# Performance work log

Measured on AMD Instinct MI355X. Metric: run time of the kernel, lower is better.

## Reference

```python
import jax, jax.numpy as jnp
import numpy as np

N_NODES = 100000
N_EDGES = 1600000
IN_DIM = 128
HEADS = 8
NEG_SLOPE = 0.2  # PyG GATConv default


def _glorot(key, shape):
    fan_in, fan_out = shape[0], shape[-1]
    lim = jnp.sqrt(6.0 / (fan_in + fan_out))
    return jax.random.uniform(key, shape, jnp.float32, -lim, lim)


def setup_inputs() -> dict:
    key = jax.random.key(0)
    ks = jax.random.split(key, 20)
    x = jax.random.normal(ks[0], (N_NODES, IN_DIM), jnp.float32)
    edge_index = jax.random.randint(ks[1], (2, N_EDGES), 0, N_NODES, jnp.int32)
    # layer 1: 128 -> 8 heads x 16
    W1 = _glorot(ks[2], (128, 128)); a_src1 = _glorot(ks[3], (8, 16)); a_dst1 = _glorot(ks[4], (8, 16)); b1 = jnp.zeros((128,), jnp.float32)
    # layer 2: 128 -> 8 heads x 16
    W2 = _glorot(ks[5], (128, 128)); a_src2 = _glorot(ks[6], (8, 16)); a_dst2 = _glorot(ks[7], (8, 16)); b2 = jnp.zeros((128,), jnp.float32)
    # layer 3: 128 -> 1 head x 64, concat=False (mean)
    W3 = _glorot(ks[8], (128, 64)); a_src3 = _glorot(ks[9], (1, 64)); a_dst3 = _glorot(ks[10], (1, 64)); b3 = jnp.zeros((64,), jnp.float32)
    Wout = _glorot(ks[11], (64, 2)); bout = jnp.zeros((2,), jnp.float32)
    return {"x": x, "edge_index": edge_index,
            "W1": W1, "a_src1": a_src1, "a_dst1": a_dst1, "b1": b1,
            "W2": W2, "a_src2": a_src2, "a_dst2": a_dst2, "b2": b2,
            "W3": W3, "a_src3": a_src3, "a_dst3": a_dst3, "b3": b3,
            "Wout": Wout, "bout": bout}


def gat_conv(x, src, dst, W, a_src, a_dst, bias, concat):
    """PyG-style GATConv (eval mode, self-loops already appended to src/dst)."""
    n = x.shape[0]
    H, C = a_src.shape
    h = (x @ W).reshape(n, H, C)                        # [N,H,C]
    alpha_src = jnp.einsum('nhc,hc->nh', h, a_src)       # [N,H]
    alpha_dst = jnp.einsum('nhc,hc->nh', h, a_dst)       # [N,H]
    e = jax.nn.leaky_relu(alpha_src[src] + alpha_dst[dst], NEG_SLOPE)  # [E,H]
    # segment softmax over incoming edges of each destination node
    m = jax.ops.segment_max(e, dst, num_segments=n)      # [N,H]
    ex = jnp.exp(e - m[dst])
    denom = jax.ops.segment_sum(ex, dst, num_segments=n)  # [N,H]
    alpha = ex / (denom[dst] + 1e-16)                    # [E,H]
    # weighted gather-scatter aggregation
    msg = alpha[:, :, None] * h[src]                     # [E,H,C]
    out = jax.ops.segment_sum(msg, dst, num_segments=n)  # [N,H,C]
    out = out.reshape(n, H * C) if concat else out.mean(axis=1)
    return out + bias


def reference(x, edge_index, W1, a_src1, a_dst1, b1, W2, a_src2, a_dst2, b2,
              W3, a_src3, a_dst3, b3, Wout, bout):
    n = x.shape[0]
    loops = jnp.arange(n, dtype=edge_index.dtype)
    src = jnp.concatenate([edge_index[0], loops])
    dst = jnp.concatenate([edge_index[1], loops])
    h = jax.nn.elu(gat_conv(x, src, dst, W1, a_src1, a_dst1, b1, concat=True))
    h = jax.nn.elu(gat_conv(h, src, dst, W2, a_src2, a_dst2, b2, concat=True))
    h = jax.nn.elu(gat_conv(h, src, dst, W3, a_src3, a_dst3, b3, concat=False))
    return h @ Wout + bout
```

## Files before the change

kernel.cpp:

```cpp
#include <hip/hip_runtime.h>
#include <math.h>

#define NN 100000
#define NE 1600000
#define ET (NE + NN)
#define SCAN_BLK 4096

__device__ inline unsigned short f2bf(float f) {
  union { float f; unsigned u; } v; v.f = f;
  unsigned r = v.u + 0x7fffu + ((v.u >> 16) & 1u);
  return (unsigned short)(r >> 16);
}
__device__ inline float bflo(unsigned u) { union { unsigned u; float f; } v; v.u = u << 16; return v.f; }
__device__ inline float bfhi(unsigned u) { union { unsigned u; float f; } v; v.u = u & 0xffff0000u; return v.f; }

__global__ __launch_bounds__(256) void k_hist(const int* __restrict__ dst, int* __restrict__ counts,
                                              int* __restrict__ slots) {
  int i = blockIdx.x * 256 + threadIdx.x;
  if (i >= ET) return;
  int d = (i < NE) ? dst[i] : (i - NE);
  slots[i] = atomicAdd(&counts[d], 1);
}

__global__ __launch_bounds__(256) void k_scan1(const int* __restrict__ counts, int* __restrict__ partial,
                                               int* __restrict__ blksum) {
  __shared__ int lds[256];
  int b = blockIdx.x, t = threadIdx.x;
  int base = b * SCAN_BLK + t * 16;
  int v[16];
  int s = 0;
#pragma unroll
  for (int j = 0; j < 16; j++) {
    int x = (base + j < NN) ? counts[base + j] : 0;
    s += x; v[j] = s;
  }
  lds[t] = s; __syncthreads();
  int tot = s;
  for (int off = 1; off < 256; off <<= 1) {
    int u = 0; if (t >= off) u = lds[t - off];
    __syncthreads(); lds[t] += u; __syncthreads();
  }
  int pre = lds[t] - tot;
#pragma unroll
  for (int j = 0; j < 16; j++) if (base + j < NN) partial[base + j] = pre + v[j];
  if (t == 255) blksum[b] = lds[255];
}

__global__ __launch_bounds__(256) void k_scan2(int* __restrict__ blksum, int nb) {
  __shared__ int lds[256];
  int t = threadIdx.x;
  int v = (t < nb) ? blksum[t] : 0;
  lds[t] = v; __syncthreads();
  for (int off = 1; off < 256; off <<= 1) {
    int u = 0; if (t >= off) u = lds[t - off];
    __syncthreads(); lds[t] += u; __syncthreads();
  }
  if (t < nb) blksum[t] = lds[t] - v;
}

__global__ __launch_bounds__(256) void k_scan3(const int* __restrict__ partial, const int* __restrict__ blksum,
                                               int* __restrict__ rowptr) {
  int i = blockIdx.x * 256 + threadIdx.x;
  if (i >= NN) return;
  rowptr[i + 1] = partial[i] + blksum[i / SCAN_BLK];
  if (i == 0) rowptr[0] = 0;
}

__global__ __launch_bounds__(256) void k_scatter(const int* __restrict__ src, const int* __restrict__ dst,
                                                 const int* __restrict__ rowptr, const int* __restrict__ slots,
                                                 int* __restrict__ esrc) {
  int i = blockIdx.x * 256 + threadIdx.x;
  if (i >= ET) return;
  int d, s;
  if (i < NE) { d = dst[i]; s = src[i]; } else { d = i - NE; s = d; }
  esrc[rowptr[d] + slots[i]] = s;
}

template<int M, bool XBF>
__global__ __launch_bounds__(256) void k_gemm(const float* __restrict__ Xf, const unsigned short* __restrict__ Xb,
                                              const float* __restrict__ W,
                                              const float* __restrict__ a_src, const float* __restrict__ a_dst,
                                              unsigned short* __restrict__ Hf, float* __restrict__ as_, float* __restrict__ ad_) {
  constexpr int CPT = M / 16;
  __shared__ float xs[64 * 36];
  __shared__ float ws[32 * M];
  const int t = threadIdx.x;
  const int tx = t & 15, ty = t >> 4;
  const int row0 = blockIdx.x * 64;
  const int c0 = tx * CPT;
  float acc[4][CPT];
#pragma unroll
  for (int i = 0; i < 4; i++)
#pragma unroll
    for (int j = 0; j < CPT; j++) acc[i][j] = 0.f;

  for (int st = 0; st < 4; ++st) {
    const int k0 = st * 32;
    __syncthreads();
    if constexpr (!XBF) {
#pragma unroll
      for (int j = 0; j < 2; ++j) {
        int flat = t + j * 256;
        int r = flat >> 3, c4 = (flat & 7) * 4;
        float4 v = make_float4(0.f, 0.f, 0.f, 0.f);
        if (row0 + r < NN) v = *(const float4*)(Xf + (size_t)(row0 + r) * 128 + k0 + c4);
        *(float4*)(xs + r * 36 + c4) = v;
      }
    } else {
      int r = t >> 2, c8 = (t & 3) * 8;
      uint4 v = make_uint4(0, 0, 0, 0);
      if (row0 + r < NN) v = *(const uint4*)(Xb + (size_t)(row0 + r) * 128 + k0 + c8);
      float* d = xs + r * 36 + c8;
      d[0] = bflo(v.x); d[1] = bfhi(v.x); d[2] = bflo(v.y); d[3] = bfhi(v.y);
      d[4] = bflo(v.z); d[5] = bfhi(v.z); d[6] = bflo(v.w); d[7] = bfhi(v.w);
    }
#pragma unroll
    for (int j = 0; j < M / 32; ++j) {
      int flat = t + j * 256;
      int r = flat / (M / 4), c4 = (flat % (M / 4)) * 4;
      *(float4*)(ws + r * M + c4) = *(const float4*)(W + (size_t)(k0 + r) * M + c4);
    }
    __syncthreads();
#pragma unroll
    for (int kk = 0; kk < 32; kk += 4) {
      float4 xv[4];
#pragma unroll
      for (int i = 0; i < 4; ++i) xv[i] = *(const float4*)(xs + (ty * 4 + i) * 36 + kk);
#pragma unroll
      for (int j = 0; j < 4; ++j) {
#pragma unroll
        for (int cc = 0; cc < CPT; cc += 4) {
          float4 wv = *(const float4*)(ws + (kk + j) * M + c0 + cc);
#pragma unroll
          for (int i = 0; i < 4; ++i) {
            float xx = ((const float*)&xv[i])[j];
            acc[i][cc + 0] += xx * wv.x;
            acc[i][cc + 1] += xx * wv.y;
            acc[i][cc + 2] += xx * wv.z;
            acc[i][cc + 3] += xx * wv.w;
          }
        }
      }
    }
  }

  float s1[4], s2[4];
#pragma unroll
  for (int i = 0; i < 4; ++i) {
    float a = 0.f, b = 0.f;
#pragma unroll
    for (int j = 0; j < CPT; ++j) { a += acc[i][j] * a_src[c0 + j]; b += acc[i][j] * a_dst[c0 + j]; }
    s1[i] = a; s2[i] = b;
  }
  if constexpr (M == 128) {
#pragma unroll
    for (int i = 0; i < 4; ++i) { s1[i] += __shfl_xor(s1[i], 1); s2[i] += __shfl_xor(s2[i], 1); }
  } else {
#pragma unroll
    for (int off = 1; off < 16; off <<= 1)
#pragma unroll
      for (int i = 0; i < 4; ++i) { s1[i] += __shfl_xor(s1[i], off); s2[i] += __shfl_xor(s2[i], off); }
  }
#pragma unroll
  for (int i = 0; i < 4; ++i) {
    int r = row0 + ty * 4 + i;
    if (r < NN) {
      if constexpr (M == 128) {
        uint4 pk;
        pk.x = (unsigned)f2bf(acc[i][0]) | ((unsigned)f2bf(acc[i][1]) << 16);
        pk.y = (unsigned)f2bf(acc[i][2]) | ((unsigned)f2bf(acc[i][3]) << 16);
        pk.z = (unsigned)f2bf(acc[i][4]) | ((unsigned)f2bf(acc[i][5]) << 16);
        pk.w = (unsigned)f2bf(acc[i][6]) | ((unsigned)f2bf(acc[i][7]) << 16);
        *(uint4*)(Hf + (size_t)r * M + c0) = pk;
        if ((tx & 1) == 0) { as_[r * 8 + (tx >> 1)] = s1[i]; ad_[r * 8 + (tx >> 1)] = s2[i]; }
      } else {
        uint2 pk;
        pk.x = (unsigned)f2bf(acc[i][0]) | ((unsigned)f2bf(acc[i][1]) << 16);
        pk.y = (unsigned)f2bf(acc[i][2]) | ((unsigned)f2bf(acc[i][3]) << 16);
        *(uint2*)(Hf + (size_t)r * M + c0) = pk;
        if (tx == 0) { as_[r] = s1[i]; ad_[r] = s2[i]; }
      }
    }
  }
}

template<int HH, int C, bool FINAL>
__global__ __launch_bounds__(256) void k_aggregate(const unsigned short* __restrict__ Hf, const float* __restrict__ as_,
                                                   const float* __restrict__ ad_, const int* __restrict__ rowptr,
                                                   const int* __restrict__ esrc, const float* __restrict__ bias,
                                                   const float* __restrict__ Wout, const float* __restrict__ bout,
                                                   unsigned short* __restrict__ outb, float* __restrict__ outf) {
  constexpr int CT = HH * C;
  constexpr int Q = CT / 4;
  int g = blockIdx.x * 256 + threadIdx.x;
  if (g >= NN * Q) return;
  int node = g / Q;
  int q = g - node * Q;
  int c = q * 4;
  int hh = c / C;
  int i0 = rowptr[node], i1 = rowptr[node + 1];
  float ad = ad_[node * HH + hh];
  float m0 = -INFINITY, d0 = 0.f;
  float m1 = -INFINITY, d1 = 0.f;
  float4 a0 = make_float4(0.f, 0.f, 0.f, 0.f);
  float4 a1 = make_float4(0.f, 0.f, 0.f, 0.f);
  int i = i0;
  for (; i + 1 < i1; i += 2) {
    int sA = esrc[i], sB = esrc[i + 1];
    float eA = as_[sA * HH + hh] + ad;
    float eB = as_[sB * HH + hh] + ad;
    uint2 hA = *(const uint2*)(Hf + (size_t)sA * CT + c);
    uint2 hB = *(const uint2*)(Hf + (size_t)sB * CT + c);
    eA = fmaxf(eA, 0.2f * eA);
    eB = fmaxf(eB, 0.2f * eB);
    float nmA = fmaxf(m0, eA), nmB = fmaxf(m1, eB);
    float scA = __expf(m0 - nmA), scB = __expf(m1 - nmB);
    float pA = __expf(eA - nmA), pB = __expf(eB - nmB);
    d0 = d0 * scA + pA;                 d1 = d1 * scB + pB;
    a0.x = a0.x * scA + pA * bflo(hA.x); a1.x = a1.x * scB + pB * bflo(hB.x);
    a0.y = a0.y * scA + pA * bfhi(hA.x); a1.y = a1.y * scB + pB * bfhi(hB.x);
    a0.z = a0.z * scA + pA * bflo(hA.y); a1.z = a1.z * scB + pB * bflo(hB.y);
    a0.w = a0.w * scA + pA * bfhi(hA.y); a1.w = a1.w * scB + pB * bfhi(hB.y);
    m0 = nmA; m1 = nmB;
  }
  if (i < i1) {
    int sA = esrc[i];
    float eA = as_[sA * HH + hh] + ad;
    uint2 hA = *(const uint2*)(Hf + (size_t)sA * CT + c);
    eA = fmaxf(eA, 0.2f * eA);
    float nmA = fmaxf(m0, eA);
    float scA = __expf(m0 - nmA);
    float pA = __expf(eA - nmA);
    d0 = d0 * scA + pA;
    a0.x = a0.x * scA + pA * bflo(hA.x);
    a0.y = a0.y * scA + pA * bfhi(hA.x);
    a0.z = a0.z * scA + pA * bflo(hA.y);
    a0.w = a0.w * scA + pA * bfhi(hA.y);
    m0 = nmA;
  }
  float mm = fmaxf(m0, m1);
  float s0 = __expf(m0 - mm), s1v = __expf(m1 - mm);
  float den = d0 * s0 + d1 * s1v;
  float4 acc;
  acc.x = a0.x * s0 + a1.x * s1v;
  acc.y = a0.y * s0 + a1.y * s1v;
  acc.z = a0.z * s0 + a1.z * s1v;
  acc.w = a0.w * s0 + a1.w * s1v;

  float inv = 1.f / den;
  float4 o;
  o.x = acc.x * inv + bias[c + 0];
  o.y = acc.y * inv + bias[c + 1];
  o.z = acc.z * inv + bias[c + 2];
  o.w = acc.w * inv + bias[c + 3];
  o.x = o.x > 0.f ? o.x : __expf(o.x) - 1.f;
  o.y = o.y > 0.f ? o.y : __expf(o.y) - 1.f;
  o.z = o.z > 0.f ? o.z : __expf(o.z) - 1.f;
  o.w = o.w > 0.f ? o.w : __expf(o.w) - 1.f;
  if constexpr (!FINAL) {
    uint2 pk;
    pk.x = (unsigned)f2bf(o.x) | ((unsigned)f2bf(o.y) << 16);
    pk.y = (unsigned)f2bf(o.z) | ((unsigned)f2bf(o.w) << 16);
    *(uint2*)(outb + (size_t)node * CT + c) = pk;
  } else {
    float p0 = o.x * Wout[(c + 0) * 2 + 0] + o.y * Wout[(c + 1) * 2 + 0]
             + o.z * Wout[(c + 2) * 2 + 0] + o.w * Wout[(c + 3) * 2 + 0];
    float p1 = o.x * Wout[(c + 0) * 2 + 1] + o.y * Wout[(c + 1) * 2 + 1]
             + o.z * Wout[(c + 2) * 2 + 1] + o.w * Wout[(c + 3) * 2 + 1];
#pragma unroll
    for (int off = 1; off < 16; off <<= 1) { p0 += __shfl_xor(p0, off); p1 += __shfl_xor(p1, off); }
    if (q == 0) { outf[node * 2 + 0] = p0 + bout[0]; outf[node * 2 + 1] = p1 + bout[1]; }
  }
}

extern "C" void kernel_launch(void* const* d_in, const int* in_sizes, int n_in,
                              void* d_out, int out_size, void* d_ws, size_t ws_size,
                              hipStream_t stream) {
  const float* x    = (const float*)d_in[0];
  const int*   ei   = (const int*)d_in[1];
  const float* W1   = (const float*)d_in[2];
  const float* as1  = (const float*)d_in[3];
  const float* ad1  = (const float*)d_in[4];
  const float* b1   = (const float*)d_in[5];
  const float* W2   = (const float*)d_in[6];
  const float* as2  = (const float*)d_in[7];
  const float* ad2  = (const float*)d_in[8];
  const float* b2   = (const float*)d_in[9];
  const float* W3   = (const float*)d_in[10];
  const float* as3  = (const float*)d_in[11];
  const float* ad3  = (const float*)d_in[12];
  const float* b3   = (const float*)d_in[13];
  const float* Wout = (const float*)d_in[14];
  const float* bout = (const float*)d_in[15];
  const int* srcp = ei;
  const int* dstp = ei + NE;

  char* p = (char*)d_ws;
  auto alloc = [&](size_t bytes) { char* r = p; p += (bytes + 255) & ~size_t(255); return r; };
  int*            rowptr  = (int*)alloc((size_t)(NN + 1) * 4);
  int*            counts  = (int*)alloc((size_t)NN * 4);
  int*            partial = (int*)alloc((size_t)NN * 4);
  int*            blksum  = (int*)alloc(256 * 4);
  int*            esrc    = (int*)alloc((size_t)ET * 4);
  int*            slots   = (int*)alloc((size_t)ET * 4);
  float*          asb     = (float*)alloc((size_t)NN * 8 * 4);
  float*          adb     = (float*)alloc((size_t)NN * 8 * 4);
  unsigned short* hfb     = (unsigned short*)alloc((size_t)NN * 128 * 2);
  unsigned short* actb    = (unsigned short*)alloc((size_t)NN * 128 * 2);

  hipMemsetAsync(counts, 0, (size_t)NN * 4, stream);
  int gE = (ET + 255) / 256;
  int nb = (NN + SCAN_BLK - 1) / SCAN_BLK;
  k_hist<<<gE, 256, 0, stream>>>(dstp, counts, slots);
  k_scan1<<<nb, 256, 0, stream>>>(counts, partial, blksum);
  k_scan2<<<1, 256, 0, stream>>>(blksum, nb);
  k_scan3<<<(NN + 255) / 256, 256, 0, stream>>>(partial, blksum, rowptr);
  k_scatter<<<gE, 256, 0, stream>>>(srcp, dstp, rowptr, slots, esrc);

  int gGemm = (NN + 63) / 64;
  k_gemm<128, false><<<gGemm, 256, 0, stream>>>(x, nullptr, W1, as1, ad1, hfb, asb, adb);
  k_aggregate<8, 16, false><<<(NN * 32 + 255) / 256, 256, 0, stream>>>(hfb, asb, adb, rowptr, esrc, b1, nullptr, nullptr, actb, nullptr);
  k_gemm<128, true><<<gGemm, 256, 0, stream>>>(nullptr, actb, W2, as2, ad2, hfb, asb, adb);
  k_aggregate<8, 16, false><<<(NN * 32 + 255) / 256, 256, 0, stream>>>(hfb, asb, adb, rowptr, esrc, b2, nullptr, nullptr, actb, nullptr);
  k_gemm<64, true><<<gGemm, 256, 0, stream>>>(nullptr, actb, W3, as3, ad3, hfb, asb, adb);
  k_aggregate<1, 64, true><<<(NN * 16 + 255) / 256, 256, 0, stream>>>(hfb, asb, adb, rowptr, esrc, b3, Wout, bout, nullptr, (float*)d_out);
}
```

Before: 466.0 us.

## Precompute softmax numerators and inverse denominators in separate per-head kernel

Adds a k_mden kernel that computes, per destination node and head, the segment max and the denominator, and stores the unnormalized exp weights per edge in bf16 along with the inverse denominator. The aggregation kernel then only gathers features and does plain FMAs, with no online-softmax rescaling or redundant exp work across the lanes of a head. In exchange it adds an extra launch per layer, a two-pass edge traversal, and a per-edge alpha buffer write and read. Storing alpha in bf16 also lowers precision.

```diff
diff --git a/kernel.cpp b/kernel.cpp
--- a/kernel.cpp
+++ b/kernel.cpp
@@ -13,6 +13,7 @@
 }
 __device__ inline float bflo(unsigned u) { union { unsigned u; float f; } v; v.u = u << 16; return v.f; }
 __device__ inline float bfhi(unsigned u) { union { unsigned u; float f; } v; v.u = u & 0xffff0000u; return v.f; }
+__device__ inline float bfs(unsigned short u) { union { unsigned u; float f; } v; v.u = ((unsigned)u) << 16; return v.f; }
 
 __global__ __launch_bounds__(256) void k_hist(const int* __restrict__ dst, int* __restrict__ counts,
                                               int* __restrict__ slots) {
@@ -184,10 +185,41 @@
   }
 }
 
+template<int HH>
+__global__ __launch_bounds__(256) void k_mden(const float* __restrict__ as_, const float* __restrict__ ad_,
+                                              const int* __restrict__ rowptr, const int* __restrict__ esrc,
+                                              unsigned short* __restrict__ alpha, float* __restrict__ invd) {
+  int g = blockIdx.x * 256 + threadIdx.x;
+  if (g >= NN * HH) return;
+  int node = g / HH;
+  int h = g - node * HH;
+  int i0 = rowptr[node], i1 = rowptr[node + 1];
+  float ad = ad_[g];
+  float m = -INFINITY;
+  for (int i = i0; i < i1; ++i) {
+    int s = esrc[i];
+    float e = as_[s * HH + h] + ad;
+    e = fmaxf(e, 0.2f * e);
+    m = fmaxf(m, e);
+  }
+  float den = 0.f;
+  for (int i = i0; i < i1; ++i) {
+    int s = esrc[i];
+    float e = as_[s * HH + h] + ad;
+    e = fmaxf(e, 0.2f * e);
+    float p = __expf(e - m);
+    den += p;
+    alpha[(size_t)i * HH + h] = f2bf(p);
+  }
+  invd[g] = 1.f / den;
+}
+
 template<int HH, int C, bool FINAL>
-__global__ __launch_bounds__(256) void k_aggregate(const unsigned short* __restrict__ Hf, const float* __restrict__ as_,
-                                                   const float* __restrict__ ad_, const int* __restrict__ rowptr,
-                                                   const int* __restrict__ esrc, const float* __restrict__ bias,
+__global__ __launch_bounds__(256) void k_aggregate(const unsigned short* __restrict__ Hf,
+                                                   const unsigned short* __restrict__ alpha,
+                                                   const float* __restrict__ invd,
+                                                   const int* __restrict__ rowptr, const int* __restrict__ esrc,
+                                                   const float* __restrict__ bias,
                                                    const float* __restrict__ Wout, const float* __restrict__ bout,
                                                    unsigned short* __restrict__ outb, float* __restrict__ outf) {
   constexpr int CT = HH * C;
@@ -199,60 +231,35 @@
   int c = q * 4;
   int hh = c / C;
   int i0 = rowptr[node], i1 = rowptr[node + 1];
-  float ad = ad_[node * HH + hh];
-  float m0 = -INFINITY, d0 = 0.f;
-  float m1 = -INFINITY, d1 = 0.f;
   float4 a0 = make_float4(0.f, 0.f, 0.f, 0.f);
   float4 a1 = make_float4(0.f, 0.f, 0.f, 0.f);
   int i = i0;
   for (; i + 1 < i1; i += 2) {
     int sA = esrc[i], sB = esrc[i + 1];
-    float eA = as_[sA * HH + hh] + ad;
-    float eB = as_[sB * HH + hh] + ad;
+    float pA = bfs(alpha[(size_t)i * HH + hh]);
+    float pB = bfs(alpha[(size_t)(i + 1) * HH + hh]);
     uint2 hA = *(const uint2*)(Hf + (size_t)sA * CT + c);
     uint2 hB = *(const uint2*)(Hf + (size_t)sB * CT + c);
-    eA = fmaxf(eA, 0.2f * eA);
-    eB = fmaxf(eB, 0.2f * eB);
-    float nmA = fmaxf(m0, eA), nmB = fmaxf(m1, eB);
-    float scA = __expf(m0 - nmA), scB = __expf(m1 - nmB);
-    float pA = __expf(eA - nmA), pB = __expf(eB - nmB);
-    d0 = d0 * scA + pA;                 d1 = d1 * scB + pB;
-    a0.x = a0.x * scA + pA * bflo(hA.x); a1.x = a1.x * scB + pB * bflo(hB.x);
-    a0.y = a0.y * scA + pA * bfhi(hA.x); a1.y = a1.y * scB + pB * bfhi(hB.x);
-    a0.z = a0.z * scA + pA * bflo(hA.y); a1.z = a1.z * scB + pB * bflo(hB.y);
-    a0.w = a0.w * scA + pA * bfhi(hA.y); a1.w = a1.w * scB + pB * bfhi(hB.y);
-    m0 = nmA; m1 = nmB;
+    a0.x = fmaf(pA, bflo(hA.x), a0.x);  a1.x = fmaf(pB, bflo(hB.x), a1.x);
+    a0.y = fmaf(pA, bfhi(hA.x), a0.y);  a1.y = fmaf(pB, bfhi(hB.x), a1.y);
+    a0.z = fmaf(pA, bflo(hA.y), a0.z);  a1.z = fmaf(pB, bflo(hB.y), a1.z);
+    a0.w = fmaf(pA, bfhi(hA.y), a0.w);  a1.w = fmaf(pB, bfhi(hB.y), a1.w);
   }
   if (i < i1) {
     int sA = esrc[i];
-    float eA = as_[sA * HH + hh] + ad;
+    float pA = bfs(alpha[(size_t)i * HH + hh]);
     uint2 hA = *(const uint2*)(Hf + (size_t)sA * CT + c);
-    eA = fmaxf(eA, 0.2f * eA);
-    float nmA = fmaxf(m0, eA);
-    float scA = __expf(m0 - nmA);
-    float pA = __expf(eA - nmA);
-    d0 = d0 * scA + pA;
-    a0.x = a0.x * scA + pA * bflo(hA.x);
-    a0.y = a0.y * scA + pA * bfhi(hA.x);
-    a0.z = a0.z * scA + pA * bflo(hA.y);
-    a0.w = a0.w * scA + pA * bfhi(hA.y);
-    m0 = nmA;
-  }
-  float mm = fmaxf(m0, m1);
-  float s0 = __expf(m0 - mm), s1v = __expf(m1 - mm);
-  float den = d0 * s0 + d1 * s1v;
-  float4 acc;
-  acc.x = a0.x * s0 + a1.x * s1v;
-  acc.y = a0.y * s0 + a1.y * s1v;
-  acc.z = a0.z * s0 + a1.z * s1v;
-  acc.w = a0.w * s0 + a1.w * s1v;
-
-  float inv = 1.f / den;
+    a0.x = fmaf(pA, bflo(hA.x), a0.x);
+    a0.y = fmaf(pA, bfhi(hA.x), a0.y);
+    a0.z = fmaf(pA, bflo(hA.y), a0.z);
+    a0.w = fmaf(pA, bfhi(hA.y), a0.w);
+  }
+  float inv = invd[node * HH + hh];
   float4 o;
-  o.x = acc.x * inv + bias[c + 0];
-  o.y = acc.y * inv + bias[c + 1];
-  o.z = acc.z * inv + bias[c + 2];
-  o.w = acc.w * inv + bias[c + 3];
+  o.x = (a0.x + a1.x) * inv + bias[c + 0];
+  o.y = (a0.y + a1.y) * inv + bias[c + 1];
+  o.z = (a0.z + a1.z) * inv + bias[c + 2];
+  o.w = (a0.w + a1.w) * inv + bias[c + 3];
   o.x = o.x > 0.f ? o.x : __expf(o.x) - 1.f;
   o.y = o.y > 0.f ? o.y : __expf(o.y) - 1.f;
   o.z = o.z > 0.f ? o.z : __expf(o.z) - 1.f;
@@ -307,6 +314,8 @@
   float*          adb     = (float*)alloc((size_t)NN * 8 * 4);
   unsigned short* hfb     = (unsigned short*)alloc((size_t)NN * 128 * 2);
   unsigned short* actb    = (unsigned short*)alloc((size_t)NN * 128 * 2);
+  unsigned short* alphab  = (unsigned short*)alloc((size_t)ET * 8 * 2);
+  float*          invdb   = (float*)alloc((size_t)NN * 8 * 4);
 
   hipMemsetAsync(counts, 0, (size_t)NN * 4, stream);
   int gE = (ET + 255) / 256;
@@ -319,9 +328,12 @@
 
   int gGemm = (NN + 63) / 64;
   k_gemm<128, false><<<gGemm, 256, 0, stream>>>(x, nullptr, W1, as1, ad1, hfb, asb, adb);
-  k_aggregate<8, 16, false><<<(NN * 32 + 255) / 256, 256, 0, stream>>>(hfb, asb, adb, rowptr, esrc, b1, nullptr, nullptr, actb, nullptr);
+  k_mden<8><<<(NN * 8 + 255) / 256, 256, 0, stream>>>(asb, adb, rowptr, esrc, alphab, invdb);
+  k_aggregate<8, 16, false><<<(NN * 32 + 255) / 256, 256, 0, stream>>>(hfb, alphab, invdb, rowptr, esrc, b1, nullptr, nullptr, actb, nullptr);
   k_gemm<128, true><<<gGemm, 256, 0, stream>>>(nullptr, actb, W2, as2, ad2, hfb, asb, adb);
-  k_aggregate<8, 16, false><<<(NN * 32 + 255) / 256, 256, 0, stream>>>(hfb, asb, adb, rowptr, esrc, b2, nullptr, nullptr, actb, nullptr);
+  k_mden<8><<<(NN * 8 + 255) / 256, 256, 0, stream>>>(asb, adb, rowptr, esrc, alphab, invdb);
+  k_aggregate<8, 16, false><<<(NN * 32 + 255) / 256, 256, 0, stream>>>(hfb, alphab, invdb, rowptr, esrc, b2, nullptr, nullptr, actb, nullptr);
   k_gemm<64, true><<<gGemm, 256, 0, stream>>>(nullptr, actb, W3, as3, ad3, hfb, asb, adb);
-  k_aggregate<1, 64, true><<<(NN * 16 + 255) / 256, 256, 0, stream>>>(hfb, asb, adb, rowptr, esrc, b3, Wout, bout, nullptr, (float*)d_out);
-}
+  k_mden<1><<<(NN + 255) / 256, 256, 0, stream>>>(asb, adb, rowptr, esrc, alphab, invdb);
+  k_aggregate<1, 64, true><<<(NN * 16 + 255) / 256, 256, 0, stream>>>(hfb, alphab, invdb, rowptr, esrc, b3, Wout, bout, nullptr, (float*)d_out);
+}
```

New measurement: 583.7 us. +25.2%, slower.
